# Performance work log

Measured on AMD Instinct MI355X. Metric: run time of the kernel, lower is better.

## Reference

```python
import jax, jax.numpy as jnp
import numpy as np

N_NODES = 50000
N_EDGES = 800000
N_GRAPHS = 512
NUM_TYPES = 1000
EMB = 128
HID = 128


def setup_inputs() -> dict:
    key = jax.random.key(0)
    ks = jax.random.split(key, 8)
    x_type = jax.random.randint(ks[0], (N_NODES,), 0, NUM_TYPES, dtype=jnp.int32)
    edge_index = jax.random.randint(ks[1], (2, N_EDGES), 0, N_NODES, dtype=jnp.int32)
    batch = jnp.sort(jax.random.randint(ks[2], (N_NODES,), 0, N_GRAPHS, dtype=jnp.int32))
    emb = jax.random.normal(ks[3], (NUM_TYPES, EMB), jnp.float32)
    s1 = 1.0 / np.sqrt(EMB)
    s2 = 1.0 / np.sqrt(HID)
    W1 = jax.random.normal(ks[4], (EMB, HID), jnp.float32) * s1
    b1 = jnp.zeros((HID,), jnp.float32)
    W2 = jax.random.normal(ks[5], (HID, HID), jnp.float32) * s2
    b2 = jnp.zeros((HID,), jnp.float32)
    return {"x_type": x_type, "edge_index": edge_index, "batch": batch,
            "emb": emb, "W1": W1, "b1": b1, "W2": W2, "b2": b2}


def _gcn_norm(edge_index, n_nodes):
    # PyG GCNConv default: add self-loops, symmetric normalization.
    loops = jnp.arange(n_nodes, dtype=edge_index.dtype)
    src = jnp.concatenate([edge_index[0], loops])  # [E+N]
    dst = jnp.concatenate([edge_index[1], loops])
    deg = jax.ops.segment_sum(jnp.ones_like(dst, jnp.float32), dst, num_segments=n_nodes)
    dis = jax.lax.rsqrt(deg)  # deg >= 1 thanks to self-loops
    norm = dis[src] * dis[dst]  # [E+N]
    return src, dst, norm


def _gcn_conv(x, src, dst, norm, W, b, n_nodes):
    h = x @ W                                  # [N, out]
    msg = h[src] * norm[:, None]               # edge-gathered, normalized messages
    out = jax.ops.segment_sum(msg, dst, num_segments=n_nodes)  # scatter-add
    return out + b


def reference(x_type, edge_index, batch, emb, W1, b1, W2, b2):
    src, dst, norm = _gcn_norm(edge_index, N_NODES)
    x = emb[x_type]                            # [N, EMB]
    x = jax.nn.relu(_gcn_conv(x, src, dst, norm, W1, b1, N_NODES))
    x = _gcn_conv(x, src, dst, norm, W2, b2, N_NODES)
    # index_add_ pooling over graphs (dropout is identity in eval / p=0)
    out = jax.ops.segment_sum(x, batch, num_segments=N_GRAPHS)  # [G, HID]
    return out
```

## Files before the change

### kernel.cpp

```cpp
#include <hip/hip_runtime.h>

#define N_NODES 50000
#define N_EDGES 800000
#define N_GRAPHS 512
#define FDIM 128
#define NTYPES_PAD 1000

#define NBLK 128
#define CHUNK ((N_EDGES + NBLK - 1) / NBLK)
#define NQUAD (N_NODES / 4)
#define NSB ((NQUAD + 255) / 256)
#define NPW 4
#define NW ((N_NODES + NPW - 1) / NPW)

typedef __bf16 bf16x8 __attribute__((ext_vector_type(8)));
typedef float f32x4 __attribute__((ext_vector_type(4)));
union BF8 { bf16x8 v; unsigned short u[8]; };

__device__ __forceinline__ unsigned short f2bf(float f) {
  unsigned int u = __float_as_uint(f);
  unsigned int r = (u + 0x7FFFu + ((u >> 16) & 1u)) >> 16;
  return (unsigned short)r;
}
__device__ __forceinline__ float bflo(unsigned int v) {
  return __uint_as_float(v << 16);
}
__device__ __forceinline__ float bfhi(unsigned int v) {
  return __uint_as_float(v & 0xFFFF0000u);
}

__global__ __launch_bounds__(512) void k_hist(const int* __restrict__ dst,
                                              unsigned int* __restrict__ Hist,
                                              unsigned char* __restrict__ rank8,
                                              int* __restrict__ g_done) {
  __shared__ unsigned int h[NQUAD];
  int b = blockIdx.x, t = threadIdx.x;
  if (b == 0 && t == 0) *g_done = 0;
  for (int i = t; i < NQUAD; i += 512) h[i] = 0;
  __syncthreads();
  int e0 = b * CHUNK, e1 = min(e0 + CHUNK, N_EDGES);
  for (int e = e0 + t; e < e1; e += 512) {
    int d = dst[e];
    unsigned int sh = (d & 3) * 8;
    unsigned int old = atomicAdd(&h[d >> 2], 1u << sh);
    rank8[e] = (unsigned char)((old >> sh) & 0xFFu);
  }
  __syncthreads();
  unsigned int* H = Hist + (size_t)b * NQUAD;
  for (int i = t; i < NQUAD; i += 512) H[i] = h[i];
}

__global__ __launch_bounds__(256) void k_prep(
    const unsigned int* __restrict__ Hist, const int* __restrict__ x_type,
    const int* __restrict__ batch, unsigned int* __restrict__ Cur,
    float* __restrict__ dis, unsigned int* __restrict__ nodeinfo,
    int* __restrict__ row_ptr, float* __restrict__ Zb,
    int* __restrict__ gstart, int* __restrict__ g_bsum,
    int* __restrict__ g_done) {
  int blk = blockIdx.x, tid = threadIdx.x;
  int q = blk * 256 + tid;
  int gt = blk * 256 + tid;

  for (int i = gt; i < N_GRAPHS * FDIM; i += NSB * 256) Zb[i] = 0.0f;

  if (q < NQUAD) {
    int i0 = 4 * q;
    int prev = (i0 == 0) ? -1 : batch[i0 - 1];
#pragma unroll
    for (int k = 0; k < 4; ++k) {
      int i = i0 + k;
      int bb = batch[i];
      for (int g = prev + 1; g <= bb; ++g) gstart[g] = i;
      prev = bb;
    }
    if (i0 + 3 == N_NODES - 1)
      for (int g = prev + 1; g <= N_GRAPHS; ++g) gstart[g] = N_NODES;
  }

  unsigned int r0 = 0, r1 = 0, r2 = 0, r3 = 0;
  if (q < NQUAD) {
    for (int b = 0; b < NBLK; ++b) {
      unsigned int v = Hist[(size_t)b * NQUAD + q];
      Cur[(size_t)b * NQUAD + q] =
          (r0 & 255u) | ((r1 & 255u) << 8) | ((r2 & 255u) << 16) | (r3 << 24);
      r0 += v & 255u;
      r1 += (v >> 8) & 255u;
      r2 += (v >> 16) & 255u;
      r3 += v >> 24;
    }
    float4 dv = make_float4(rsqrtf((float)r0 + 1.f), rsqrtf((float)r1 + 1.f),
                            rsqrtf((float)r2 + 1.f), rsqrtf((float)r3 + 1.f));
    ((float4*)dis)[q] = dv;
    int4 xt = ((const int4*)x_type)[q];
    ((uint4*)nodeinfo)[q] = make_uint4(
        (unsigned int)xt.x | (r0 << 16), (unsigned int)xt.y | (r1 << 16),
        (unsigned int)xt.z | (r2 << 16), (unsigned int)xt.w | (r3 << 16));
  }

  int tsum = (q < NQUAD) ? (int)(r0 + r1 + r2 + r3) : 0;
  __shared__ int s[256];
  s[tid] = tsum;
  __syncthreads();
  for (int d = 1; d < 256; d <<= 1) {
    int u = (tid >= d) ? s[tid - d] : 0;
    __syncthreads();
    s[tid] += u;
    __syncthreads();
  }
  int excl = s[tid] - tsum;
  int btotal = s[255];

  if (tid == 0) {
    atomicExch(&g_bsum[blk], btotal);
    __threadfence();
    atomicAdd(g_done, 1);
    while (atomicAdd(g_done, 0) < NSB) {
    }
  }
  __syncthreads();
  __shared__ int sb[NSB];
  if (tid < NSB) sb[tid] = atomicAdd(&g_bsum[tid], 0);
  __syncthreads();
  int bpref = 0;
  for (int t = 0; t < blk; ++t) bpref += sb[t];

  if (q < NQUAD) {
    int base = bpref + excl;
    ((int4*)row_ptr)[q] =
        make_int4(base, base + (int)r0, base + (int)(r0 + r1),
                  base + (int)(r0 + r1 + r2));
  }
  if (q == NQUAD - 1) row_ptr[N_NODES] = N_EDGES;
}

__global__ __launch_bounds__(512) void k_fill2(
    const int* __restrict__ src, const int* __restrict__ dst,
    const int* __restrict__ row_ptr, const unsigned int* __restrict__ Cur,
    const unsigned char* __restrict__ rank8,
    const unsigned int* __restrict__ nodeinfo, unsigned int* __restrict__ csr1,
    unsigned short* __restrict__ csr2) {
  int e = blockIdx.x * blockDim.x + threadIdx.x;
  if (e >= N_EDGES) return;
  int b = e / CHUNK;
  int s = src[e], d = dst[e];
  unsigned int cw = Cur[(size_t)b * NQUAD + (d >> 2)];
  int base = (int)((cw >> ((d & 3) * 8)) & 0xFFu);
  int pos = row_ptr[d] + base + (int)rank8[e];
  csr1[pos] = nodeinfo[s];
  csr2[pos] = (unsigned short)s;
}

__global__ __launch_bounds__(256) void k_embw(
    const float* __restrict__ emb, const float* __restrict__ W1,
    unsigned short* __restrict__ T1) {
  __shared__ unsigned short Ws[128 * 128];
  int t = threadIdx.x, w = t >> 6, l = t & 63;
  for (int i = t; i < 16384; i += 256) {
    int k = i >> 7, n = i & 127;
    Ws[n * 128 + (k ^ ((n & 15) << 3))] = f2bf(W1[i]);
  }
  int row0 = blockIdx.x * 64 + w * 16;
  int arow = row0 + (l & 15);
  bool ok = arow < NTYPES_PAD;
  bf16x8 a[4];
#pragma unroll
  for (int ks = 0; ks < 4; ++ks) {
    BF8 av;
    const float* ap = emb + (size_t)arow * FDIM + (l >> 4) * 8 + ks * 32;
#pragma unroll
    for (int i = 0; i < 8; ++i) av.u[i] = ok ? f2bf(ap[i]) : 0;
    a[ks] = av.v;
  }
  __syncthreads();
  f32x4 acc[8] = {};
#pragma unroll
  for (int ks = 0; ks < 4; ++ks) {
#pragma unroll
    for (int ct = 0; ct < 8; ++ct) {
      int n = ct * 16 + (l & 15);
      int kk = (ks * 32 + (l >> 4) * 8) ^ ((n & 15) << 3);
      bf16x8 b = *(const bf16x8*)&Ws[n * 128 + kk];
      acc[ct] =
          __builtin_amdgcn_mfma_f32_16x16x32_bf16(a[ks], b, acc[ct], 0, 0, 0);
    }
  }
#pragma unroll
  for (int ct = 0; ct < 8; ++ct) {
    int col = ct * 16 + (l & 15);
#pragma unroll
    for (int r = 0; r < 4; ++r) {
      int row = row0 + (l >> 4) * 4 + r;
      if (row < NTYPES_PAD) T1[row * FDIM + col] = f2bf(acc[ct][r]);
    }
  }
}

__global__ void k_agg1(const unsigned int* __restrict__ nodeinfo,
                       const unsigned short* __restrict__ T1,
                       const float* __restrict__ b1,
                       const int* __restrict__ row_ptr,
                       const unsigned int* __restrict__ csr1,
                       const float* __restrict__ dis,
                       unsigned int* __restrict__ y1) {
  int gid = blockIdx.x * blockDim.x + threadIdx.x;
  int node = gid >> 6;
  int lane = gid & 63;
  if (node >= N_NODES) return;
  const unsigned int* T = (const unsigned int*)T1;
  float di = dis[node];
  unsigned int ni = nodeinfo[node];
  unsigned int v = T[(size_t)(ni & 0xFFFFu) * 64 + lane];
  float ax = bflo(v) * di, ay = bfhi(v) * di;
  int j = row_ptr[node], end = row_ptr[node + 1];
  for (; j + 8 <= end; j += 8) {
    unsigned int e0 = csr1[j], e1 = csr1[j + 1];
    unsigned int e2 = csr1[j + 2], e3 = csr1[j + 3];
    unsigned int e4 = csr1[j + 4], e5 = csr1[j + 5];
    unsigned int e6 = csr1[j + 6], e7 = csr1[j + 7];
    unsigned int u0 = T[(size_t)(e0 & 0xFFFFu) * 64 + lane];
    unsigned int u1 = T[(size_t)(e1 & 0xFFFFu) * 64 + lane];
    unsigned int u2 = T[(size_t)(e2 & 0xFFFFu) * 64 + lane];
    unsigned int u3 = T[(size_t)(e3 & 0xFFFFu) * 64 + lane];
    unsigned int u4 = T[(size_t)(e4 & 0xFFFFu) * 64 + lane];
    unsigned int u5 = T[(size_t)(e5 & 0xFFFFu) * 64 + lane];
    unsigned int u6 = T[(size_t)(e6 & 0xFFFFu) * 64 + lane];
    unsigned int u7 = T[(size_t)(e7 & 0xFFFFu) * 64 + lane];
    float n0 = rsqrtf((float)(e0 >> 16) + 1.f);
    float n1 = rsqrtf((float)(e1 >> 16) + 1.f);
    float n2 = rsqrtf((float)(e2 >> 16) + 1.f);
    float n3 = rsqrtf((float)(e3 >> 16) + 1.f);
    float n4 = rsqrtf((float)(e4 >> 16) + 1.f);
    float n5 = rsqrtf((float)(e5 >> 16) + 1.f);
    float n6 = rsqrtf((float)(e6 >> 16) + 1.f);
    float n7 = rsqrtf((float)(e7 >> 16) + 1.f);
    ax = fmaf(bflo(u0), n0, ax); ay = fmaf(bfhi(u0), n0, ay);
    ax = fmaf(bflo(u1), n1, ax); ay = fmaf(bfhi(u1), n1, ay);
    ax = fmaf(bflo(u2), n2, ax); ay = fmaf(bfhi(u2), n2, ay);
    ax = fmaf(bflo(u3), n3, ax); ay = fmaf(bfhi(u3), n3, ay);
    ax = fmaf(bflo(u4), n4, ax); ay = fmaf(bfhi(u4), n4, ay);
    ax = fmaf(bflo(u5), n5, ax); ay = fmaf(bfhi(u5), n5, ay);
    ax = fmaf(bflo(u6), n6, ax); ay = fmaf(bfhi(u6), n6, ay);
    ax = fmaf(bflo(u7), n7, ax); ay = fmaf(bfhi(u7), n7, ay);
  }
  for (; j < end; ++j) {
    unsigned int e = csr1[j];
    unsigned int u = T[(size_t)(e & 0xFFFFu) * 64 + lane];
    float nw = rsqrtf((float)(e >> 16) + 1.f);
    ax = fmaf(bflo(u), nw, ax);
    ay = fmaf(bfhi(u), nw, ay);
  }
  float2 bb = ((const float2*)b1)[lane];
  ax = fmaxf(fmaf(di, ax, bb.x), 0.f) * di;
  ay = fmaxf(fmaf(di, ay, bb.y), 0.f) * di;
  y1[(size_t)node * 64 + lane] = (unsigned int)f2bf(ax) |
                                 ((unsigned int)f2bf(ay) << 16);
}

__global__ void k_aggpool(const unsigned int* __restrict__ y1,
                          const int* __restrict__ row_ptr,
                          const unsigned short* __restrict__ csr2,
                          const float* __restrict__ dis,
                          const int* __restrict__ batch,
                          float* __restrict__ Partials, int* __restrict__ Gid,
                          float* __restrict__ Zb) {
  int gid = blockIdx.x * blockDim.x + threadIdx.x;
  int wid = gid >> 6;
  int lane = gid & 63;
  int n0 = wid * NPW;
  if (n0 >= N_NODES) return;
  int nend = min(n0 + NPW, N_NODES);
  int g0 = batch[n0];
  int gcur = g0;
  float px = 0.f, py = 0.f;
  float ax = 0.f, ay = 0.f;
  for (int node = n0; node < nend; ++node) {
    int g = batch[node];
    if (g != gcur) {
      if (gcur == g0) {
        px = ax; py = ay;
      } else {
        atomicAdd(&Zb[(size_t)gcur * FDIM + 2 * lane], ax);
        atomicAdd(&Zb[(size_t)gcur * FDIM + 2 * lane + 1], ay);
      }
      ax = 0.f; ay = 0.f;
      gcur = g;
    }
    float di = dis[node];
    unsigned int v = y1[(size_t)node * 64 + lane];
    float sx = bflo(v), sy = bfhi(v);
    int j = row_ptr[node], end = row_ptr[node + 1];
    for (; j + 8 <= end; j += 8) {
      int s0 = csr2[j], s1 = csr2[j + 1], s2 = csr2[j + 2], s3 = csr2[j + 3];
      int s4 = csr2[j + 4], s5 = csr2[j + 5], s6 = csr2[j + 6], s7 = csr2[j + 7];
      unsigned int u0 = y1[(size_t)s0 * 64 + lane];
      unsigned int u1 = y1[(size_t)s1 * 64 + lane];
      unsigned int u2 = y1[(size_t)s2 * 64 + lane];
      unsigned int u3 = y1[(size_t)s3 * 64 + lane];
      unsigned int u4 = y1[(size_t)s4 * 64 + lane];
      unsigned int u5 = y1[(size_t)s5 * 64 + lane];
      unsigned int u6 = y1[(size_t)s6 * 64 + lane];
      unsigned int u7 = y1[(size_t)s7 * 64 + lane];
      sx += bflo(u0) + bflo(u1) + bflo(u2) + bflo(u3);
      sy += bfhi(u0) + bfhi(u1) + bfhi(u2) + bfhi(u3);
      sx += bflo(u4) + bflo(u5) + bflo(u6) + bflo(u7);
      sy += bfhi(u4) + bfhi(u5) + bfhi(u6) + bfhi(u7);
    }
    for (; j < end; ++j) {
      unsigned int u = y1[(size_t)csr2[j] * 64 + lane];
      sx += bflo(u);
      sy += bfhi(u);
    }
    ax = fmaf(di, sx, ax);
    ay = fmaf(di, sy, ay);
  }
  if (gcur == g0) {
    px = ax; py = ay;
  } else {
    atomicAdd(&Zb[(size_t)gcur * FDIM + 2 * lane], ax);
    atomicAdd(&Zb[(size_t)gcur * FDIM + 2 * lane + 1], ay);
  }
  ((float2*)Partials)[(size_t)wid * 64 + lane] = make_float2(px, py);
  if (lane == 0) Gid[wid] = g0;
}

__global__ __launch_bounds__(128) void k_poolzw2(
    const float* __restrict__ Partials, const int* __restrict__ Gid,
    const float* __restrict__ Zb, const int* __restrict__ gstart,
    const float* __restrict__ W2, const float* __restrict__ b2,
    float* __restrict__ out) {
  __shared__ float Zs[FDIM];
  int g = blockIdx.x, t = threadIdx.x;
  int s = gstart[g], e = gstart[g + 1];
  float acc = Zb[(size_t)g * FDIM + t];
  if (e > s) {
    int w0 = s / NPW, w1 = (e - 1) / NPW;
    for (int w = w0; w <= w1; ++w)
      if (Gid[w] == g) acc += Partials[(size_t)w * FDIM + t];
  }
  Zs[t] = acc;
  __syncthreads();
  float o = 0.f;
#pragma unroll 8
  for (int k = 0; k < FDIM; ++k) o = fmaf(Zs[k], W2[k * FDIM + t], o);
  out[(size_t)g * FDIM + t] = o + (float)(e - s) * b2[t];
}

extern "C" void kernel_launch(void* const* d_in, const int* in_sizes, int n_in,
                              void* d_out, int out_size, void* d_ws,
                              size_t ws_size, hipStream_t stream) {
  const int* x_type = (const int*)d_in[0];
  const int* edge_index = (const int*)d_in[1];
  const int* batch = (const int*)d_in[2];
  const float* emb = (const float*)d_in[3];
  const float* W1 = (const float*)d_in[4];
  const float* b1 = (const float*)d_in[5];
  const float* W2 = (const float*)d_in[6];
  const float* b2 = (const float*)d_in[7];
  float* out = (float*)d_out;

  const int* src = edge_index;
  const int* dst = edge_index + N_EDGES;

  char* p = (char*)d_ws;
  size_t off = 0;
  auto alloc = [&](size_t bytes) {
    void* r = p + off;
    off = (off + bytes + 255) & ~(size_t)255;
    return r;
  };
  float* dis = (float*)alloc(N_NODES * 4);
  int* row_ptr = (int*)alloc((N_NODES + 1) * 4);
  int* gstart = (int*)alloc((N_GRAPHS + 1) * 4);
  unsigned int* nodeinfo = (unsigned int*)alloc(N_NODES * 4);
  unsigned int* Hist = (unsigned int*)alloc((size_t)NBLK * NQUAD * 4);
  unsigned int* Cur = (unsigned int*)alloc((size_t)NBLK * NQUAD * 4);
  unsigned char* rank8 = (unsigned char*)alloc(N_EDGES);
  unsigned int* csr1 = (unsigned int*)alloc((size_t)N_EDGES * 4);
  unsigned short* csr2 = (unsigned short*)alloc((size_t)N_EDGES * 2);
  unsigned short* T1 = (unsigned short*)alloc((size_t)NTYPES_PAD * FDIM * 2);
  unsigned int* y1 = (unsigned int*)alloc((size_t)N_NODES * 64 * 4);
  float* Partials = (float*)alloc((size_t)NW * FDIM * 4);
  int* Gid = (int*)alloc(NW * 4);
  float* Zb = (float*)alloc((size_t)N_GRAPHS * FDIM * 4);
  int* g_bsum = (int*)alloc(NSB * 4);
  int* g_done = (int*)alloc(4);
  (void)ws_size;

  k_hist<<<NBLK, 512, 0, stream>>>(dst, Hist, rank8, g_done);
  k_prep<<<NSB, 256, 0, stream>>>(Hist, x_type, batch, Cur, dis, nodeinfo,
                                  row_ptr, Zb, gstart, g_bsum, g_done);
  k_fill2<<<(N_EDGES + 511) / 512, 512, 0, stream>>>(
      src, dst, row_ptr, Cur, rank8, nodeinfo, csr1, csr2);
  k_embw<<<(NTYPES_PAD + 63) / 64, 256, 0, stream>>>(emb, W1, T1);
  k_agg1<<<(N_NODES * 64 + 255) / 256, 256, 0, stream>>>(
      nodeinfo, T1, b1, row_ptr, csr1, dis, y1);
  k_aggpool<<<(NW * 64 + 255) / 256, 256, 0, stream>>>(
      y1, row_ptr, csr2, dis, batch, Partials, Gid, Zb);
  k_poolzw2<<<N_GRAPHS, 128, 0, stream>>>(Partials, Gid, Zb, gstart, W2, b2,
                                          out);
}
```

Measured before the change: 162.9 us.

## Pack CSR into 64-bit entries with source, type and destination norm

Replaces the two CSR arrays (packed type+degree word and 16-bit source) with one 64-bit entry per edge holding source id, source type and bf16 destination norm. Layer 1 now reads the source norm from the dis array instead of computing rsqrt from degree, and layer 2 applies per-edge weights. Layer 2 also merges consecutive same-graph nodes into a single CSR range with deeper unrolling. k_prep switches to 128-thread blocks and no longer builds nodeinfo. The cost is doubled CSR bytes, an extra dis gather per edge in layer 1, and bf16 rounding of the norm in layer 2.

```diff
diff --git a/kernel.cpp b/kernel.cpp
--- a/kernel.cpp
+++ b/kernel.cpp
@@ -9,7 +9,7 @@
 #define NBLK 128
 #define CHUNK ((N_EDGES + NBLK - 1) / NBLK)
 #define NQUAD (N_NODES / 4)
-#define NSB ((NQUAD + 255) / 256)
+#define NSB ((NQUAD + 127) / 128)
 #define NPW 4
 #define NW ((N_NODES + NPW - 1) / NPW)
 
@@ -50,18 +50,17 @@
   for (int i = t; i < NQUAD; i += 512) H[i] = h[i];
 }
 
-__global__ __launch_bounds__(256) void k_prep(
-    const unsigned int* __restrict__ Hist, const int* __restrict__ x_type,
-    const int* __restrict__ batch, unsigned int* __restrict__ Cur,
-    float* __restrict__ dis, unsigned int* __restrict__ nodeinfo,
+__global__ __launch_bounds__(128) void k_prep(
+    const unsigned int* __restrict__ Hist, const int* __restrict__ batch,
+    unsigned int* __restrict__ Cur, float* __restrict__ dis,
     int* __restrict__ row_ptr, float* __restrict__ Zb,
     int* __restrict__ gstart, int* __restrict__ g_bsum,
     int* __restrict__ g_done) {
   int blk = blockIdx.x, tid = threadIdx.x;
-  int q = blk * 256 + tid;
-  int gt = blk * 256 + tid;
-
-  for (int i = gt; i < N_GRAPHS * FDIM; i += NSB * 256) Zb[i] = 0.0f;
+  int q = blk * 128 + tid;
+
+  for (int i = blk * 128 + tid; i < N_GRAPHS * FDIM; i += NSB * 128)
+    Zb[i] = 0.0f;
 
   if (q < NQUAD) {
     int i0 = 4 * q;
@@ -91,24 +90,20 @@
     float4 dv = make_float4(rsqrtf((float)r0 + 1.f), rsqrtf((float)r1 + 1.f),
                             rsqrtf((float)r2 + 1.f), rsqrtf((float)r3 + 1.f));
     ((float4*)dis)[q] = dv;
-    int4 xt = ((const int4*)x_type)[q];
-    ((uint4*)nodeinfo)[q] = make_uint4(
-        (unsigned int)xt.x | (r0 << 16), (unsigned int)xt.y | (r1 << 16),
-        (unsigned int)xt.z | (r2 << 16), (unsigned int)xt.w | (r3 << 16));
   }
 
   int tsum = (q < NQUAD) ? (int)(r0 + r1 + r2 + r3) : 0;
-  __shared__ int s[256];
+  __shared__ int s[128];
   s[tid] = tsum;
   __syncthreads();
-  for (int d = 1; d < 256; d <<= 1) {
+  for (int d = 1; d < 128; d <<= 1) {
     int u = (tid >= d) ? s[tid - d] : 0;
     __syncthreads();
     s[tid] += u;
     __syncthreads();
   }
   int excl = s[tid] - tsum;
-  int btotal = s[255];
+  int btotal = s[127];
 
   if (tid == 0) {
     atomicExch(&g_bsum[blk], btotal);
@@ -135,10 +130,9 @@
 
 __global__ __launch_bounds__(512) void k_fill2(
     const int* __restrict__ src, const int* __restrict__ dst,
-    const int* __restrict__ row_ptr, const unsigned int* __restrict__ Cur,
-    const unsigned char* __restrict__ rank8,
-    const unsigned int* __restrict__ nodeinfo, unsigned int* __restrict__ csr1,
-    unsigned short* __restrict__ csr2) {
+    const int* __restrict__ x_type, const int* __restrict__ row_ptr,
+    const unsigned int* __restrict__ Cur, const unsigned char* __restrict__ rank8,
+    const float* __restrict__ dis, unsigned long long* __restrict__ csr) {
   int e = blockIdx.x * blockDim.x + threadIdx.x;
   if (e >= N_EDGES) return;
   int b = e / CHUNK;
@@ -146,8 +140,9 @@
   unsigned int cw = Cur[(size_t)b * NQUAD + (d >> 2)];
   int base = (int)((cw >> ((d & 3) * 8)) & 0xFFu);
   int pos = row_ptr[d] + base + (int)rank8[e];
-  csr1[pos] = nodeinfo[s];
-  csr2[pos] = (unsigned short)s;
+  unsigned int lo = (unsigned int)s | ((unsigned int)x_type[s] << 16);
+  unsigned int hi = (unsigned int)f2bf(dis[d]);
+  csr[pos] = (unsigned long long)lo | ((unsigned long long)hi << 32);
 }
 
 __global__ __launch_bounds__(256) void k_embw(
@@ -195,11 +190,11 @@
   }
 }
 
-__global__ void k_agg1(const unsigned int* __restrict__ nodeinfo,
+__global__ void k_agg1(const int* __restrict__ x_type,
                        const unsigned short* __restrict__ T1,
                        const float* __restrict__ b1,
                        const int* __restrict__ row_ptr,
-                       const unsigned int* __restrict__ csr1,
+                       const unsigned long long* __restrict__ csr,
                        const float* __restrict__ dis,
                        unsigned int* __restrict__ y1) {
   int gid = blockIdx.x * blockDim.x + threadIdx.x;
@@ -207,32 +202,28 @@
   int lane = gid & 63;
   if (node >= N_NODES) return;
   const unsigned int* T = (const unsigned int*)T1;
+  const unsigned int* C = (const unsigned int*)csr;
   float di = dis[node];
-  unsigned int ni = nodeinfo[node];
-  unsigned int v = T[(size_t)(ni & 0xFFFFu) * 64 + lane];
+  unsigned int v = T[(size_t)x_type[node] * 64 + lane];
   float ax = bflo(v) * di, ay = bfhi(v) * di;
   int j = row_ptr[node], end = row_ptr[node + 1];
   for (; j + 8 <= end; j += 8) {
-    unsigned int e0 = csr1[j], e1 = csr1[j + 1];
-    unsigned int e2 = csr1[j + 2], e3 = csr1[j + 3];
-    unsigned int e4 = csr1[j + 4], e5 = csr1[j + 5];
-    unsigned int e6 = csr1[j + 6], e7 = csr1[j + 7];
-    unsigned int u0 = T[(size_t)(e0 & 0xFFFFu) * 64 + lane];
-    unsigned int u1 = T[(size_t)(e1 & 0xFFFFu) * 64 + lane];
-    unsigned int u2 = T[(size_t)(e2 & 0xFFFFu) * 64 + lane];
-    unsigned int u3 = T[(size_t)(e3 & 0xFFFFu) * 64 + lane];
-    unsigned int u4 = T[(size_t)(e4 & 0xFFFFu) * 64 + lane];
-    unsigned int u5 = T[(size_t)(e5 & 0xFFFFu) * 64 + lane];
-    unsigned int u6 = T[(size_t)(e6 & 0xFFFFu) * 64 + lane];
-    unsigned int u7 = T[(size_t)(e7 & 0xFFFFu) * 64 + lane];
-    float n0 = rsqrtf((float)(e0 >> 16) + 1.f);
-    float n1 = rsqrtf((float)(e1 >> 16) + 1.f);
-    float n2 = rsqrtf((float)(e2 >> 16) + 1.f);
-    float n3 = rsqrtf((float)(e3 >> 16) + 1.f);
-    float n4 = rsqrtf((float)(e4 >> 16) + 1.f);
-    float n5 = rsqrtf((float)(e5 >> 16) + 1.f);
-    float n6 = rsqrtf((float)(e6 >> 16) + 1.f);
-    float n7 = rsqrtf((float)(e7 >> 16) + 1.f);
+    unsigned int e0 = C[2 * j], e1 = C[2 * j + 2];
+    unsigned int e2 = C[2 * j + 4], e3 = C[2 * j + 6];
+    unsigned int e4 = C[2 * j + 8], e5 = C[2 * j + 10];
+    unsigned int e6 = C[2 * j + 12], e7 = C[2 * j + 14];
+    unsigned int u0 = T[(size_t)(e0 >> 16) * 64 + lane];
+    unsigned int u1 = T[(size_t)(e1 >> 16) * 64 + lane];
+    unsigned int u2 = T[(size_t)(e2 >> 16) * 64 + lane];
+    unsigned int u3 = T[(size_t)(e3 >> 16) * 64 + lane];
+    unsigned int u4 = T[(size_t)(e4 >> 16) * 64 + lane];
+    unsigned int u5 = T[(size_t)(e5 >> 16) * 64 + lane];
+    unsigned int u6 = T[(size_t)(e6 >> 16) * 64 + lane];
+    unsigned int u7 = T[(size_t)(e7 >> 16) * 64 + lane];
+    float n0 = dis[e0 & 0xFFFFu], n1 = dis[e1 & 0xFFFFu];
+    float n2 = dis[e2 & 0xFFFFu], n3 = dis[e3 & 0xFFFFu];
+    float n4 = dis[e4 & 0xFFFFu], n5 = dis[e5 & 0xFFFFu];
+    float n6 = dis[e6 & 0xFFFFu], n7 = dis[e7 & 0xFFFFu];
     ax = fmaf(bflo(u0), n0, ax); ay = fmaf(bfhi(u0), n0, ay);
     ax = fmaf(bflo(u1), n1, ax); ay = fmaf(bfhi(u1), n1, ay);
     ax = fmaf(bflo(u2), n2, ax); ay = fmaf(bfhi(u2), n2, ay);
@@ -242,10 +233,24 @@
     ax = fmaf(bflo(u6), n6, ax); ay = fmaf(bfhi(u6), n6, ay);
     ax = fmaf(bflo(u7), n7, ax); ay = fmaf(bfhi(u7), n7, ay);
   }
+  for (; j + 4 <= end; j += 4) {
+    unsigned int e0 = C[2 * j], e1 = C[2 * j + 2];
+    unsigned int e2 = C[2 * j + 4], e3 = C[2 * j + 6];
+    unsigned int u0 = T[(size_t)(e0 >> 16) * 64 + lane];
+    unsigned int u1 = T[(size_t)(e1 >> 16) * 64 + lane];
+    unsigned int u2 = T[(size_t)(e2 >> 16) * 64 + lane];
+    unsigned int u3 = T[(size_t)(e3 >> 16) * 64 + lane];
+    float n0 = dis[e0 & 0xFFFFu], n1 = dis[e1 & 0xFFFFu];
+    float n2 = dis[e2 & 0xFFFFu], n3 = dis[e3 & 0xFFFFu];
+    ax = fmaf(bflo(u0), n0, ax); ay = fmaf(bfhi(u0), n0, ay);
+    ax = fmaf(bflo(u1), n1, ax); ay = fmaf(bfhi(u1), n1, ay);
+    ax = fmaf(bflo(u2), n2, ax); ay = fmaf(bfhi(u2), n2, ay);
+    ax = fmaf(bflo(u3), n3, ax); ay = fmaf(bfhi(u3), n3, ay);
+  }
   for (; j < end; ++j) {
-    unsigned int e = csr1[j];
-    unsigned int u = T[(size_t)(e & 0xFFFFu) * 64 + lane];
-    float nw = rsqrtf((float)(e >> 16) + 1.f);
+    unsigned int e = C[2 * j];
+    unsigned int u = T[(size_t)(e >> 16) * 64 + lane];
+    float nw = dis[e & 0xFFFFu];
     ax = fmaf(bflo(u), nw, ax);
     ay = fmaf(bfhi(u), nw, ay);
   }
@@ -258,7 +263,7 @@
 
 __global__ void k_aggpool(const unsigned int* __restrict__ y1,
                           const int* __restrict__ row_ptr,
-                          const unsigned short* __restrict__ csr2,
+                          const unsigned long long* __restrict__ csr,
                           const float* __restrict__ dis,
                           const int* __restrict__ batch,
                           float* __restrict__ Partials, int* __restrict__ Gid,
@@ -270,54 +275,55 @@
   if (n0 >= N_NODES) return;
   int nend = min(n0 + NPW, N_NODES);
   int g0 = batch[n0];
-  int gcur = g0;
   float px = 0.f, py = 0.f;
-  float ax = 0.f, ay = 0.f;
-  for (int node = n0; node < nend; ++node) {
+  int node = n0;
+  while (node < nend) {
     int g = batch[node];
-    if (g != gcur) {
-      if (gcur == g0) {
-        px = ax; py = ay;
-      } else {
-        atomicAdd(&Zb[(size_t)gcur * FDIM + 2 * lane], ax);
-        atomicAdd(&Zb[(size_t)gcur * FDIM + 2 * lane + 1], ay);
+    int rend = node + 1;
+    while (rend < nend && batch[rend] == g) ++rend;
+    float sx = 0.f, sy = 0.f;
+    for (int n = node; n < rend; ++n) {
+      float dn = dis[n];
+      unsigned int v = y1[(size_t)n * 64 + lane];
+      sx = fmaf(dn, bflo(v), sx);
+      sy = fmaf(dn, bfhi(v), sy);
+    }
+    int j = row_ptr[node], jend = row_ptr[rend];
+    for (; j + 16 <= jend; j += 16) {
+#pragma unroll
+      for (int k = 0; k < 16; ++k) {
+        unsigned long long e = csr[j + k];
+        unsigned int u = y1[(size_t)(e & 0xFFFFu) * 64 + lane];
+        float w = __uint_as_float(((unsigned int)(e >> 32)) << 16);
+        sx = fmaf(bflo(u), w, sx);
+        sy = fmaf(bfhi(u), w, sy);
       }
-      ax = 0.f; ay = 0.f;
-      gcur = g;
-    }
-    float di = dis[node];
-    unsigned int v = y1[(size_t)node * 64 + lane];
-    float sx = bflo(v), sy = bfhi(v);
-    int j = row_ptr[node], end = row_ptr[node + 1];
-    for (; j + 8 <= end; j += 8) {
-      int s0 = csr2[j], s1 = csr2[j + 1], s2 = csr2[j + 2], s3 = csr2[j + 3];
-      int s4 = csr2[j + 4], s5 = csr2[j + 5], s6 = csr2[j + 6], s7 = csr2[j + 7];
-      unsigned int u0 = y1[(size_t)s0 * 64 + lane];
-      unsigned int u1 = y1[(size_t)s1 * 64 + lane];
-      unsigned int u2 = y1[(size_t)s2 * 64 + lane];
-      unsigned int u3 = y1[(size_t)s3 * 64 + lane];
-      unsigned int u4 = y1[(size_t)s4 * 64 + lane];
-      unsigned int u5 = y1[(size_t)s5 * 64 + lane];
-      unsigned int u6 = y1[(size_t)s6 * 64 + lane];
-      unsigned int u7 = y1[(size_t)s7 * 64 + lane];
-      sx += bflo(u0) + bflo(u1) + bflo(u2) + bflo(u3);
-      sy += bfhi(u0) + bfhi(u1) + bfhi(u2) + bfhi(u3);
-      sx += bflo(u4) + bflo(u5) + bflo(u6) + bflo(u7);
-      sy += bfhi(u4) + bfhi(u5) + bfhi(u6) + bfhi(u7);
-    }
-    for (; j < end; ++j) {
-      unsigned int u = y1[(size_t)csr2[j] * 64 + lane];
-      sx += bflo(u);
-      sy += bfhi(u);
-    }
-    ax = fmaf(di, sx, ax);
-    ay = fmaf(di, sy, ay);
-  }
-  if (gcur == g0) {
-    px = ax; py = ay;
-  } else {
-    atomicAdd(&Zb[(size_t)gcur * FDIM + 2 * lane], ax);
-    atomicAdd(&Zb[(size_t)gcur * FDIM + 2 * lane + 1], ay);
+    }
+    for (; j + 4 <= jend; j += 4) {
+#pragma unroll
+      for (int k = 0; k < 4; ++k) {
+        unsigned long long e = csr[j + k];
+        unsigned int u = y1[(size_t)(e & 0xFFFFu) * 64 + lane];
+        float w = __uint_as_float(((unsigned int)(e >> 32)) << 16);
+        sx = fmaf(bflo(u), w, sx);
+        sy = fmaf(bfhi(u), w, sy);
+      }
+    }
+    for (; j < jend; ++j) {
+      unsigned long long e = csr[j];
+      unsigned int u = y1[(size_t)(e & 0xFFFFu) * 64 + lane];
+      float w = __uint_as_float(((unsigned int)(e >> 32)) << 16);
+      sx = fmaf(bflo(u), w, sx);
+      sy = fmaf(bfhi(u), w, sy);
+    }
+    if (g == g0) {
+      px += sx;
+      py += sy;
+    } else {
+      atomicAdd(&Zb[(size_t)g * FDIM + 2 * lane], sx);
+      atomicAdd(&Zb[(size_t)g * FDIM + 2 * lane + 1], sy);
+    }
+    node = rend;
   }
   ((float2*)Partials)[(size_t)wid * 64 + lane] = make_float2(px, py);
   if (lane == 0) Gid[wid] = g0;
@@ -371,12 +377,11 @@
   float* dis = (float*)alloc(N_NODES * 4);
   int* row_ptr = (int*)alloc((N_NODES + 1) * 4);
   int* gstart = (int*)alloc((N_GRAPHS + 1) * 4);
-  unsigned int* nodeinfo = (unsigned int*)alloc(N_NODES * 4);
   unsigned int* Hist = (unsigned int*)alloc((size_t)NBLK * NQUAD * 4);
   unsigned int* Cur = (unsigned int*)alloc((size_t)NBLK * NQUAD * 4);
   unsigned char* rank8 = (unsigned char*)alloc(N_EDGES);
-  unsigned int* csr1 = (unsigned int*)alloc((size_t)N_EDGES * 4);
-  unsigned short* csr2 = (unsigned short*)alloc((size_t)N_EDGES * 2);
+  unsigned long long* csr =
+      (unsigned long long*)alloc((size_t)N_EDGES * 8);
   unsigned short* T1 = (unsigned short*)alloc((size_t)NTYPES_PAD * FDIM * 2);
   unsigned int* y1 = (unsigned int*)alloc((size_t)N_NODES * 64 * 4);
   float* Partials = (float*)alloc((size_t)NW * FDIM * 4);
@@ -387,15 +392,15 @@
   (void)ws_size;
 
   k_hist<<<NBLK, 512, 0, stream>>>(dst, Hist, rank8, g_done);
-  k_prep<<<NSB, 256, 0, stream>>>(Hist, x_type, batch, Cur, dis, nodeinfo,
-                                  row_ptr, Zb, gstart, g_bsum, g_done);
+  k_prep<<<NSB, 128, 0, stream>>>(Hist, batch, Cur, dis, row_ptr, Zb, gstart,
+                                  g_bsum, g_done);
   k_fill2<<<(N_EDGES + 511) / 512, 512, 0, stream>>>(
-      src, dst, row_ptr, Cur, rank8, nodeinfo, csr1, csr2);
+      src, dst, x_type, row_ptr, Cur, rank8, dis, csr);
   k_embw<<<(NTYPES_PAD + 63) / 64, 256, 0, stream>>>(emb, W1, T1);
   k_agg1<<<(N_NODES * 64 + 255) / 256, 256, 0, stream>>>(
-      nodeinfo, T1, b1, row_ptr, csr1, dis, y1);
+      x_type, T1, b1, row_ptr, csr, dis, y1);
   k_aggpool<<<(NW * 64 + 255) / 256, 256, 0, stream>>>(
-      y1, row_ptr, csr2, dis, batch, Partials, Gid, Zb);
+      y1, row_ptr, csr, dis, batch, Partials, Gid, Zb);
   k_poolzw2<<<N_GRAPHS, 128, 0, stream>>>(Partials, Gid, Zb, gstart, W2, b2,
                                           out);
 }
```

Measured after the change: 151.3 us. 1.08x faster.
